# Performance work log

Hardware: AMD Instinct MI355X
Metric: run time of the kernel (lower is better)

The kernel has to match this reference:

```python
import jax, jax.numpy as jnp
import numpy as np

TEMPERATURE = 0.5


def setup_inputs() -> dict:
    key = jax.random.key(0)
    k1, k2 = jax.random.split(key)
    N, D = 4096, 256
    emb_i = jax.random.normal(k1, (N, D), dtype=jnp.float32)
    emb_j = jax.random.normal(k2, (N, D), dtype=jnp.float32)
    return {"emb_i": emb_i, "emb_j": emb_j, "batch_size": N}


def reference(emb_i, emb_j, batch_size):
    N = batch_size
    # L2-normalize each embedding row (F.normalize eps=1e-12)
    def l2n(x):
        return x / jnp.maximum(jnp.linalg.norm(x, axis=1, keepdims=True), 1e-12)
    reps = jnp.concatenate([l2n(emb_i), l2n(emb_j)], axis=0)  # [2N, D]
    # cosine similarity of normalized vectors == dot product
    logits = (reps @ reps.T) / TEMPERATURE                    # [2N, 2N]
    twoN = 2 * N
    # denominator excludes only the self term k != i (stable logsumexp)
    diag_mask = jnp.eye(twoN, dtype=bool)
    masked = jnp.where(diag_mask, -jnp.inf, logits)
    log_denom = jax.nn.logsumexp(masked, axis=1)              # [2N]
    # positive pair for row i is (i+N) mod 2N
    idx = jnp.arange(twoN)
    pos = logits[idx, (idx + N) % twoN]                       # [2N]
    # loss = 1/(2N) * sum_i -log(exp(pos_i)/denom_i)
    return jnp.mean(log_denom - pos)
```

## Files before the change

### kernel.cpp

```cpp
#include <hip/hip_runtime.h>

typedef short short8 __attribute__((ext_vector_type(8)));
typedef float f32x4  __attribute__((ext_vector_type(4)));

#define TWO_N 8192
#define NHALF 4096
#define DDIM  256

__device__ __forceinline__ float b2f(unsigned short u) {
    return __uint_as_float(((unsigned int)u) << 16);
}
__device__ __forceinline__ unsigned short f2b(float f) {
    unsigned int u = __float_as_uint(f);
    u += 0x7fffu + ((u >> 16) & 1u);
    return (unsigned short)(u >> 16);
}

__device__ __forceinline__ int probe_is_f32(const void* p, int lane) {
    unsigned int u = ((const unsigned int*)p)[lane];
    float lowv = __uint_as_float(u << 16);
    int crazy = !(fabsf(lowv) <= 1024.0f);
    return __ballot(crazy) != 0ull;
}

typedef __attribute__((address_space(1))) const unsigned int guint_t;
typedef __attribute__((address_space(3))) unsigned int luint_t;
__device__ __forceinline__ void gl_lds16(const unsigned short* g, unsigned short* l) {
    __builtin_amdgcn_global_load_lds((guint_t*)(const void*)g, (luint_t*)(void*)l, 16, 0, 0);
}

__global__ __launch_bounds__(256) void k_norm(const void* __restrict__ ei,
                                              const void* __restrict__ ej,
                                              unsigned short* __restrict__ reps) {
    int row  = (blockIdx.x * 256 + threadIdx.x) >> 6;
    int lane = threadIdx.x & 63;
    int isf  = probe_is_f32(ei, lane);
    int first = (row < NHALF);
    int r     = first ? row : row - NHALF;
    float x0, x1, x2, x3;
    if (isf) {
        const float* s = (first ? (const float*)ei : (const float*)ej) + (size_t)r * DDIM;
        float4 v = ((const float4*)s)[lane];
        x0 = v.x; x1 = v.y; x2 = v.z; x3 = v.w;
    } else {
        const unsigned short* s =
            (first ? (const unsigned short*)ei : (const unsigned short*)ej) + (size_t)r * DDIM;
        ushort4 v = ((const ushort4*)s)[lane];
        x0 = b2f(v.x); x1 = b2f(v.y); x2 = b2f(v.z); x3 = b2f(v.w);
    }
    float ss = x0 * x0 + x1 * x1 + x2 * x2 + x3 * x3;
    for (int off = 32; off > 0; off >>= 1) ss += __shfl_xor(ss, off);
    float inv = 1.0f / fmaxf(sqrtf(ss), 1e-12f);
    ushort4 o;
    o.x = f2b(x0 * inv); o.y = f2b(x1 * inv);
    o.z = f2b(x2 * inv); o.w = f2b(x3 * inv);
    ((ushort4*)(reps + (size_t)row * DDIM))[lane] = o;
}

__global__ __launch_bounds__(256, 4) void k_main(const unsigned short* __restrict__ R,
                                                 float* __restrict__ S_part,
                                                 float* __restrict__ pos) {
    __shared__ __align__(16) unsigned short As[128 * 64];
    __shared__ __align__(16) unsigned short Bs[128 * 64];

    int b = blockIdx.x;
    int rb = (int)((129.0f - sqrtf(16641.0f - 8.0f * (float)b)) * 0.5f);
    if (rb > 63) rb = 63;
    while ((129 * (rb + 1) - (rb + 1) * (rb + 1)) / 2 <= b) ++rb;
    while ((129 * rb - rb * rb) / 2 > b) --rb;
    int cb = rb + (b - (129 * rb - rb * rb) / 2);

    const int tid  = threadIdx.x;
    const int wave = tid >> 6;
    const int lane = tid & 63;
    const int quad = lane >> 4;
    const int l16  = lane & 15;
    const int wr   = (wave >> 1) * 64;
    const int wc   = (wave & 1) * 64;
    const int r8   = lane >> 3;
    const int c8   = (lane & 7) ^ r8;

    f32x4 acc[4][4];
#pragma unroll
    for (int r = 0; r < 4; ++r)
#pragma unroll
        for (int c = 0; c < 4; ++c) {
            acc[r][c][0] = 0.0f; acc[r][c][1] = 0.0f;
            acc[r][c][2] = 0.0f; acc[r][c][3] = 0.0f;
        }

    for (int kc = 0; kc < 4; ++kc) {
        __syncthreads();
#pragma unroll
        for (int t = 0; t < 4; ++t) {
            int u = wave * 4 + t;
            const unsigned short* ga =
                R + (size_t)(rb * 128 + u * 8 + r8) * DDIM + kc * 64 + c8 * 8;
            const unsigned short* gb =
                R + (size_t)(cb * 128 + u * 8 + r8) * DDIM + kc * 64 + c8 * 8;
            gl_lds16(ga, &As[u * 512]);
            gl_lds16(gb, &Bs[u * 512]);
        }
        __syncthreads();

#pragma unroll
        for (int kk = 0; kk < 2; ++kk) {
            short8 afr[4], bfr[4];
            int q = kk * 4 + quad;
            int sl = q ^ (l16 & 7);
#pragma unroll
            for (int r = 0; r < 4; ++r)
                afr[r] = *(const short8*)(&As[(wr + r * 16 + l16) * 64 + sl * 8]);
#pragma unroll
            for (int c = 0; c < 4; ++c)
                bfr[c] = *(const short8*)(&Bs[(wc + c * 16 + l16) * 64 + sl * 8]);
#pragma unroll
            for (int r = 0; r < 4; ++r)
#pragma unroll
                for (int c = 0; c < 4; ++c)
                    acc[r][c] = __builtin_amdgcn_mfma_f32_16x16x32_bf16(
                        afr[r], bfr[c], acc[r][c], 0, 0, 0);
        }
    }

    float col_acc[4] = {0.0f, 0.0f, 0.0f, 0.0f};
#pragma unroll
    for (int r = 0; r < 4; ++r)
#pragma unroll
        for (int j = 0; j < 4; ++j) {
            float s = 0.0f;
#pragma unroll
            for (int c = 0; c < 4; ++c) {
                float e = __expf(fmaf(acc[r][c][j], 2.0f, -2.0f));
                s += e;
                col_acc[c] += e;
            }
            s += __shfl_xor(s, 1);
            s += __shfl_xor(s, 2);
            s += __shfl_xor(s, 4);
            s += __shfl_xor(s, 8);
            if (l16 == 0) {
                int row = rb * 128 + wr + r * 16 + quad * 4 + j;
                S_part[(size_t)(2 * cb + (wave & 1)) * TWO_N + row] = s;
            }
        }
    if (rb != cb) {
#pragma unroll
        for (int c = 0; c < 4; ++c) {
            float s = col_acc[c];
            s += __shfl_xor(s, 16);
            s += __shfl_xor(s, 32);
            if (lane < 16) {
                int row = cb * 128 + wc + c * 16 + lane;
                S_part[(size_t)(2 * rb + (wave >> 1)) * TWO_N + row] = s;
            }
        }
    }
    if (cb == rb + 32 && wr == wc) {
#pragma unroll
        for (int r = 0; r < 4; ++r)
#pragma unroll
            for (int j = 0; j < 4; ++j)
                if (quad * 4 + j == l16)
                    pos[rb * 128 + wr + r * 16 + l16] = 2.0f * acc[r][r][j];
    }
}

__global__ __launch_bounds__(256) void k_rows(const float* __restrict__ S_part,
                                              const float* __restrict__ pos,
                                              float* __restrict__ part_blk) {
    __shared__ float red[256];
    int tid = threadIdx.x;
    int rr  = tid & 63;
    int cg  = tid >> 6;
    int row = blockIdx.x * 64 + rr;
    float s = 0.0f;
#pragma unroll 8
    for (int c = cg * 32; c < cg * 32 + 32; ++c)
        s += S_part[(size_t)c * TWO_N + row];
    red[tid] = s;
    __syncthreads();
    if (tid < 64) {
        float total = red[tid] + red[tid + 64] + red[tid + 128] + red[tid + 192];
        float p = (row < NHALF) ? pos[row] : pos[row - NHALF];
        float part = 2.0f + logf(total - 1.0f) - p;
        for (int off = 32; off > 0; off >>= 1) part += __shfl_xor(part, off);
        if (tid == 0) part_blk[blockIdx.x] = part;
    }
}

__global__ __launch_bounds__(128) void k_fin(const float* __restrict__ part_blk,
                                             unsigned int* __restrict__ out) {
    int tid = threadIdx.x;
    float local = part_blk[tid];
    __shared__ float red2[2];
    for (int off = 32; off > 0; off >>= 1) local += __shfl_xor(local, off);
    if ((tid & 63) == 0) red2[tid >> 6] = local;
    __syncthreads();
    if (tid == 0) {
        float L = (red2[0] + red2[1]) / 8192.0f;
        unsigned int bb = (unsigned int)f2b(L);
        out[0] = (bb << 16) | bb;
    }
}

extern "C" void kernel_launch(void* const* d_in, const int* in_sizes, int n_in,
                              void* d_out, int out_size, void* d_ws, size_t ws_size,
                              hipStream_t stream) {
    (void)in_sizes; (void)n_in; (void)out_size; (void)ws_size;
    const void* ei = d_in[0];
    const void* ej = d_in[1];
    char* ws = (char*)d_ws;

    float*          pos      = (float*)(ws);
    float*          part_blk = (float*)(ws + 16384);
    unsigned short* reps     = (unsigned short*)(ws + 49152);
    float*          S_part   = (float*)(ws + 4243456);

    k_norm<<<2048, 256, 0, stream>>>(ei, ej, reps);
    k_main<<<2080, 256, 0, stream>>>(reps, S_part, pos);
    k_rows<<<128,  256, 0, stream>>>(S_part, pos, part_blk);
    k_fin <<<1,    128, 0, stream>>>(part_blk, (unsigned int*)d_out);
}
```

Before: 98.57 us.

## Enlarge GEMM tiles to 256x256 with double-buffered LDS and swizzled block order

The similarity kernel moves from 128x128 tiles with 256 threads to 256x256 tiles with 512 threads, each wave computing a 128x64 sub-tile. LDS staging becomes double-buffered, so the next K-chunk is prefetched while MFMAs run on the current one. Block IDs are also remapped across the triangle of tile pairs. The aim is more data reuse per loaded byte and overlap of global loads with compute. The cost is 128KB of LDS per block, higher register pressure, and only 528 blocks, which may give poor occupancy and a load-imbalance tail across the CUs.

```diff
diff --git a/kernel.cpp b/kernel.cpp
--- a/kernel.cpp
+++ b/kernel.cpp
@@ -6,6 +6,8 @@
 #define TWO_N 8192
 #define NHALF 4096
 #define DDIM  256
+#define NB    32
+#define NBLK2 528
 
 __device__ __forceinline__ float b2f(unsigned short u) {
     return __uint_as_float(((unsigned int)u) << 16);
@@ -57,75 +59,83 @@
     ((ushort4*)(reps + (size_t)row * DDIM))[lane] = o;
 }
 
-__global__ __launch_bounds__(256, 4) void k_main(const unsigned short* __restrict__ R,
+__global__ __launch_bounds__(512, 2) void k_main(const unsigned short* __restrict__ R,
                                                  float* __restrict__ S_part,
                                                  float* __restrict__ pos) {
-    __shared__ __align__(16) unsigned short As[128 * 64];
-    __shared__ __align__(16) unsigned short Bs[128 * 64];
-
-    int b = blockIdx.x;
-    int rb = (int)((129.0f - sqrtf(16641.0f - 8.0f * (float)b)) * 0.5f);
-    if (rb > 63) rb = 63;
-    while ((129 * (rb + 1) - (rb + 1) * (rb + 1)) / 2 <= b) ++rb;
-    while ((129 * rb - rb * rb) / 2 > b) --rb;
-    int cb = rb + (b - (129 * rb - rb * rb) / 2);
+    __shared__ __align__(16) unsigned short As[2][256 * 64];
+    __shared__ __align__(16) unsigned short Bs[2][256 * 64];
+
+    int b = ((int)blockIdx.x & 7) * 66 + ((int)blockIdx.x >> 3);
+    int rb = (int)((65.0f - sqrtf(4225.0f - 8.0f * (float)b)) * 0.5f);
+    if (rb > 31) rb = 31;
+    while ((65 * (rb + 1) - (rb + 1) * (rb + 1)) / 2 <= b) ++rb;
+    while ((65 * rb - rb * rb) / 2 > b) --rb;
+    int cb = rb + (b - (65 * rb - rb * rb) / 2);
 
     const int tid  = threadIdx.x;
     const int wave = tid >> 6;
     const int lane = tid & 63;
     const int quad = lane >> 4;
     const int l16  = lane & 15;
-    const int wr   = (wave >> 1) * 64;
-    const int wc   = (wave & 1) * 64;
+    const int wrg  = wave >> 2;
+    const int wcg  = wave & 3;
+    const int wr   = wrg * 128;
+    const int wc   = wcg * 64;
     const int r8   = lane >> 3;
     const int c8   = (lane & 7) ^ r8;
 
-    f32x4 acc[4][4];
-#pragma unroll
-    for (int r = 0; r < 4; ++r)
+    f32x4 acc[8][4];
+#pragma unroll
+    for (int r = 0; r < 8; ++r)
 #pragma unroll
         for (int c = 0; c < 4; ++c) {
             acc[r][c][0] = 0.0f; acc[r][c][1] = 0.0f;
             acc[r][c][2] = 0.0f; acc[r][c][3] = 0.0f;
         }
 
-    for (int kc = 0; kc < 4; ++kc) {
-        __syncthreads();
+    auto stage = [&](int d, int kc) {
 #pragma unroll
         for (int t = 0; t < 4; ++t) {
             int u = wave * 4 + t;
             const unsigned short* ga =
-                R + (size_t)(rb * 128 + u * 8 + r8) * DDIM + kc * 64 + c8 * 8;
+                R + (size_t)(rb * 256 + u * 8 + r8) * DDIM + kc * 64 + c8 * 8;
             const unsigned short* gb =
-                R + (size_t)(cb * 128 + u * 8 + r8) * DDIM + kc * 64 + c8 * 8;
-            gl_lds16(ga, &As[u * 512]);
-            gl_lds16(gb, &Bs[u * 512]);
-        }
-        __syncthreads();
-
+                R + (size_t)(cb * 256 + u * 8 + r8) * DDIM + kc * 64 + c8 * 8;
+            gl_lds16(ga, &As[d][u * 512]);
+            gl_lds16(gb, &Bs[d][u * 512]);
+        }
+    };
+
+    stage(0, 0);
+    __syncthreads();
+
+    for (int kc = 0; kc < 4; ++kc) {
+        const int cur = kc & 1;
+        if (kc < 3) stage(cur ^ 1, kc + 1);
 #pragma unroll
         for (int kk = 0; kk < 2; ++kk) {
-            short8 afr[4], bfr[4];
-            int q = kk * 4 + quad;
+            short8 afr[8], bfr[4];
+            int q  = kk * 4 + quad;
             int sl = q ^ (l16 & 7);
 #pragma unroll
-            for (int r = 0; r < 4; ++r)
-                afr[r] = *(const short8*)(&As[(wr + r * 16 + l16) * 64 + sl * 8]);
+            for (int r = 0; r < 8; ++r)
+                afr[r] = *(const short8*)(&As[cur][(wr + r * 16 + l16) * 64 + sl * 8]);
 #pragma unroll
             for (int c = 0; c < 4; ++c)
-                bfr[c] = *(const short8*)(&Bs[(wc + c * 16 + l16) * 64 + sl * 8]);
-#pragma unroll
-            for (int r = 0; r < 4; ++r)
+                bfr[c] = *(const short8*)(&Bs[cur][(wc + c * 16 + l16) * 64 + sl * 8]);
+#pragma unroll
+            for (int r = 0; r < 8; ++r)
 #pragma unroll
                 for (int c = 0; c < 4; ++c)
                     acc[r][c] = __builtin_amdgcn_mfma_f32_16x16x32_bf16(
                         afr[r], bfr[c], acc[r][c], 0, 0, 0);
         }
-    }
-
-    float col_acc[4] = {0.0f, 0.0f, 0.0f, 0.0f};
-#pragma unroll
-    for (int r = 0; r < 4; ++r)
+        if (kc < 3) __syncthreads();
+    }
+
+    float col_acc[4][2] = {{0.0f, 0.0f}, {0.0f, 0.0f}, {0.0f, 0.0f}, {0.0f, 0.0f}};
+#pragma unroll
+    for (int r = 0; r < 8; ++r)
 #pragma unroll
         for (int j = 0; j < 4; ++j) {
             float s = 0.0f;
@@ -133,36 +143,42 @@
             for (int c = 0; c < 4; ++c) {
                 float e = __expf(fmaf(acc[r][c][j], 2.0f, -2.0f));
                 s += e;
-                col_acc[c] += e;
+                col_acc[c][r >> 2] += e;
             }
             s += __shfl_xor(s, 1);
             s += __shfl_xor(s, 2);
             s += __shfl_xor(s, 4);
             s += __shfl_xor(s, 8);
             if (l16 == 0) {
-                int row = rb * 128 + wr + r * 16 + quad * 4 + j;
-                S_part[(size_t)(2 * cb + (wave & 1)) * TWO_N + row] = s;
+                int row = rb * 256 + wr + r * 16 + quad * 4 + j;
+                S_part[(size_t)(4 * cb + wcg) * TWO_N + row] = s;
             }
         }
     if (rb != cb) {
 #pragma unroll
-        for (int c = 0; c < 4; ++c) {
-            float s = col_acc[c];
-            s += __shfl_xor(s, 16);
-            s += __shfl_xor(s, 32);
-            if (lane < 16) {
-                int row = cb * 128 + wc + c * 16 + lane;
-                S_part[(size_t)(2 * rb + (wave >> 1)) * TWO_N + row] = s;
+        for (int c = 0; c < 4; ++c)
+#pragma unroll
+            for (int h = 0; h < 2; ++h) {
+                float s = col_acc[c][h];
+                s += __shfl_xor(s, 16);
+                s += __shfl_xor(s, 32);
+                if (lane < 16) {
+                    int row = cb * 256 + wc + c * 16 + lane;
+                    S_part[(size_t)(4 * rb + 2 * wrg + h) * TWO_N + row] = s;
+                }
             }
-        }
-    }
-    if (cb == rb + 32 && wr == wc) {
-#pragma unroll
-        for (int r = 0; r < 4; ++r)
-#pragma unroll
-            for (int j = 0; j < 4; ++j)
-                if (quad * 4 + j == l16)
-                    pos[rb * 128 + wr + r * 16 + l16] = 2.0f * acc[r][r][j];
+    }
+    if (cb == rb + 16) {
+        int dlt = (wc - wr) >> 4;
+#pragma unroll
+        for (int r = 0; r < 8; ++r)
+#pragma unroll
+            for (int c = 0; c < 4; ++c)
+                if (r == c + dlt)
+#pragma unroll
+                    for (int j = 0; j < 4; ++j)
+                        if (quad * 4 + j == l16)
+                            pos[rb * 256 + wr + r * 16 + l16] = 2.0f * acc[r][c][j];
     }
 }
 
@@ -218,7 +234,7 @@
     float*          S_part   = (float*)(ws + 4243456);
 
     k_norm<<<2048, 256, 0, stream>>>(ei, ej, reps);
-    k_main<<<2080, 256, 0, stream>>>(reps, S_part, pos);
+    k_main<<<NBLK2, 512, 0, stream>>>(reps, S_part, pos);
     k_rows<<<128,  256, 0, stream>>>(S_part, pos, part_blk);
     k_fin <<<1,    128, 0, stream>>>(part_blk, (unsigned int*)d_out);
 }
```

After: 115.0 us. 16.7% more time.

## Load MFMA fragments directly from global memory instead of staging through LDS

Applied to the files above, without the earlier changes.

Removes the shared-memory tiles, the global_load_lds staging and both block barriers per K chunk. Each wave now reads its A and B bf16 fragments straight from global memory, relying on L1/L2 cache for reuse across waves, and the K loop is fully unrolled. This drops barrier and LDS overhead and lets the compiler issue all loads early. The cost is redundant global/L2 traffic, since the tile is shared by two waves, and higher register pressure now that the occupancy hint is removed from launch bounds.

```diff
diff --git a/kernel.cpp b/kernel.cpp
--- a/kernel.cpp
+++ b/kernel.cpp
@@ -21,12 +21,6 @@
     float lowv = __uint_as_float(u << 16);
     int crazy = !(fabsf(lowv) <= 1024.0f);
     return __ballot(crazy) != 0ull;
-}
-
-typedef __attribute__((address_space(1))) const unsigned int guint_t;
-typedef __attribute__((address_space(3))) unsigned int luint_t;
-__device__ __forceinline__ void gl_lds16(const unsigned short* g, unsigned short* l) {
-    __builtin_amdgcn_global_load_lds((guint_t*)(const void*)g, (luint_t*)(void*)l, 16, 0, 0);
 }
 
 __global__ __launch_bounds__(256) void k_norm(const void* __restrict__ ei,
@@ -57,13 +51,10 @@
     ((ushort4*)(reps + (size_t)row * DDIM))[lane] = o;
 }
 
-__global__ __launch_bounds__(256, 4) void k_main(const unsigned short* __restrict__ R,
-                                                 float* __restrict__ S_part,
-                                                 float* __restrict__ pos) {
-    __shared__ __align__(16) unsigned short As[128 * 64];
-    __shared__ __align__(16) unsigned short Bs[128 * 64];
-
-    int b = blockIdx.x;
+__global__ __launch_bounds__(256) void k_main(const unsigned short* __restrict__ R,
+                                              float* __restrict__ S_part,
+                                              float* __restrict__ pos) {
+    int b = (int)blockIdx.x;
     int rb = (int)((129.0f - sqrtf(16641.0f - 8.0f * (float)b)) * 0.5f);
     if (rb > 63) rb = 63;
     while ((129 * (rb + 1) - (rb + 1) * (rb + 1)) / 2 <= b) ++rb;
@@ -77,8 +68,9 @@
     const int l16  = lane & 15;
     const int wr   = (wave >> 1) * 64;
     const int wc   = (wave & 1) * 64;
-    const int r8   = lane >> 3;
-    const int c8   = (lane & 7) ^ r8;
+
+    const unsigned short* Ab = R + (size_t)(rb * 128 + wr + l16) * DDIM;
+    const unsigned short* Bb = R + (size_t)(cb * 128 + wc + l16) * DDIM;
 
     f32x4 acc[4][4];
 #pragma unroll
@@ -89,31 +81,18 @@
             acc[r][c][2] = 0.0f; acc[r][c][3] = 0.0f;
         }
 
+#pragma unroll
     for (int kc = 0; kc < 4; ++kc) {
-        __syncthreads();
-#pragma unroll
-        for (int t = 0; t < 4; ++t) {
-            int u = wave * 4 + t;
-            const unsigned short* ga =
-                R + (size_t)(rb * 128 + u * 8 + r8) * DDIM + kc * 64 + c8 * 8;
-            const unsigned short* gb =
-                R + (size_t)(cb * 128 + u * 8 + r8) * DDIM + kc * 64 + c8 * 8;
-            gl_lds16(ga, &As[u * 512]);
-            gl_lds16(gb, &Bs[u * 512]);
-        }
-        __syncthreads();
-
 #pragma unroll
         for (int kk = 0; kk < 2; ++kk) {
+            const int ko = kc * 64 + (kk * 4 + quad) * 8;
             short8 afr[4], bfr[4];
-            int q = kk * 4 + quad;
-            int sl = q ^ (l16 & 7);
 #pragma unroll
             for (int r = 0; r < 4; ++r)
-                afr[r] = *(const short8*)(&As[(wr + r * 16 + l16) * 64 + sl * 8]);
+                afr[r] = *(const short8*)(Ab + (size_t)r * 16 * DDIM + ko);
 #pragma unroll
             for (int c = 0; c < 4; ++c)
-                bfr[c] = *(const short8*)(&Bs[(wc + c * 16 + l16) * 64 + sl * 8]);
+                bfr[c] = *(const short8*)(Bb + (size_t)c * 16 * DDIM + ko);
 #pragma unroll
             for (int r = 0; r < 4; ++r)
 #pragma unroll
```

New measurement: 142.8 us. 1.45x slower.
